# Kernel tuning notes

Hardware: AMD Instinct MI355X
Metric: run time of the kernel (lower is better)

The kernel has to match this reference:

```python
import jax, jax.numpy as jnp
import numpy as np

N_HEAD = 16
HEAD_DIM = 128

def rotate_half(x):
    x1, x2 = jnp.split(x, 2, axis=-1)
    return jnp.concatenate((-x2, x1), axis=-1)

def setup_inputs() -> dict:
    key = jax.random.key(0)
    ks = jax.random.split(key, 5)
    B, T, C = 2, 2048, 2048
    x = jax.random.normal(ks[0], (B, T, C), dtype=jnp.float32)
    # rotary tables as used by the module: cos/sin of shape [T, head_dim]
    pos = jnp.arange(T, dtype=jnp.float32)[:, None]
    inv_freq = 1.0 / (10000.0 ** (jnp.arange(0, HEAD_DIM, 2, dtype=jnp.float32) / HEAD_DIM))
    freqs = pos * inv_freq[None, :]            # [T, head_dim/2]
    emb = jnp.concatenate([freqs, freqs], -1)  # [T, head_dim]
    cos = jnp.cos(emb)
    sin = jnp.sin(emb)
    W_qkv = jax.random.normal(ks[1], (C, 3 * C), dtype=jnp.float32) * (C ** -0.5)
    W_proj = jax.random.normal(ks[2], (C, C), dtype=jnp.float32) * (C ** -0.5)
    return {"x": x, "cos": cos, "sin": sin, "W_qkv": W_qkv, "W_proj": W_proj}

def reference(x, cos, sin, W_qkv, W_proj):
    B, T, C = x.shape
    H, D = N_HEAD, HEAD_DIM
    qkv = x @ W_qkv                                   # [B,T,3C]
    q, k, v = jnp.split(qkv, 3, axis=2)
    # [B,T,C] -> [B,H,T,D]
    q = q.reshape(B, T, H, D).transpose(0, 2, 1, 3)
    k = k.reshape(B, T, H, D).transpose(0, 2, 1, 3)
    v = v.reshape(B, T, H, D).transpose(0, 2, 1, 3)
    c = cos[None, None, :, :]                          # [1,1,T,D]
    s = sin[None, None, :, :]
    q = q * c + rotate_half(q) * s
    k = k * c + rotate_half(k) * s
    scale = 1.0 / jnp.sqrt(jnp.float32(D))
    scores = jnp.einsum('bhqd,bhkd->bhqk', q, k) * scale
    attn = jax.nn.softmax(scores, axis=-1)
    y = jnp.einsum('bhqk,bhkd->bhqd', attn, v)         # [B,H,T,D]
    y = y.transpose(0, 2, 1, 3).reshape(B, T, C)
    return y @ W_proj
```

## Files before the change

### kernel.cpp

```cpp
#include <hip/hip_runtime.h>
#include <cstdint>
#include <cstddef>

typedef __bf16 bf16_t;
typedef __bf16 bf16x8 __attribute__((ext_vector_type(8)));
typedef __bf16 bf16x4 __attribute__((ext_vector_type(4)));
typedef float f32x4 __attribute__((ext_vector_type(4)));

#define MFMA16(a, b, c) __builtin_amdgcn_mfma_f32_16x16x32_bf16(a, b, c, 0, 0, 0)

__device__ __forceinline__ void gll16(const bf16_t* g, bf16_t* l) {
  __builtin_amdgcn_global_load_lds(
      (__attribute__((address_space(1))) uint32_t*)((uintptr_t)g),
      (__attribute__((address_space(3))) uint32_t*)((uint32_t)(uintptr_t)l),
      16, 0, 0);
}

__global__ void fill_diag(uint32_t* out, int n_u32) {
  int i = blockIdx.x * 256 + threadIdx.x;
  if (i < n_u32) out[i] = 0x447A0000u;
}

__global__ void conv_vec_f32(const float* __restrict__ in, bf16_t* __restrict__ out,
                             int n8) {
  const int i = blockIdx.x * 256 + threadIdx.x;
  if (i >= n8) return;
  const float* p = in + (size_t)i * 8;
  const f32x4 a = *(const f32x4*)p;
  const f32x4 b = *(const f32x4*)(p + 4);
  bf16x8 o;
#pragma unroll
  for (int j = 0; j < 4; ++j) {
    o[j] = (bf16_t)a[j];
    o[4 + j] = (bf16_t)b[j];
  }
  ((bf16x8*)out)[i] = o;
}

__global__ __launch_bounds__(256) void conv_transpose_f32(
    const float* __restrict__ in, bf16_t* __restrict__ out, int R, int C) {
  __shared__ bf16_t tile[64][72];
  const int bc = blockIdx.x * 64;
  const int br = blockIdx.y * 64;
  const int t = threadIdx.x;
  const int r = t >> 3;
  const int c8 = (t & 7) * 8;
#pragma unroll
  for (int ii = 0; ii < 2; ++ii) {
    const int rr = r + ii * 32;
    const float* p = in + (size_t)(br + rr) * C + bc + c8;
    const f32x4 a = *(const f32x4*)p;
    const f32x4 b = *(const f32x4*)(p + 4);
    bf16x8 v;
#pragma unroll
    for (int j = 0; j < 4; ++j) {
      v[j] = (bf16_t)a[j];
      v[4 + j] = (bf16_t)b[j];
    }
    *(bf16x8*)(&tile[rr][c8]) = v;
  }
  __syncthreads();
#pragma unroll
  for (int ii = 0; ii < 2; ++ii) {
    const int rr = r + ii * 32;
    bf16x8 o;
#pragma unroll
    for (int jj = 0; jj < 8; ++jj) o[jj] = tile[c8 + jj][rr];
    *(bf16x8*)(out + (size_t)(bc + rr) * R + br + c8) = o;
  }
}

#define MF8(MLO, AARR, BARR, NLO)                                           \
  do {                                                                      \
    _Pragma("unroll") for (int m_ = 0; m_ < 4; ++m_) {                      \
      _Pragma("unroll") for (int n_ = 0; n_ < 2; ++n_) {                    \
        acc[(MLO) + m_][(NLO) + n_] =                                       \
            MFMA16(AARR[m_][0], BARR[n_][0], acc[(MLO) + m_][(NLO) + n_]);  \
        acc[(MLO) + m_][(NLO) + n_] =                                       \
            MFMA16(AARR[m_][1], BARR[n_][1], acc[(MLO) + m_][(NLO) + n_]);  \
      }                                                                     \
    }                                                                       \
  } while (0)

template <bool C32>
__global__ __launch_bounds__(512, 2) void gemm8(
    const bf16_t* __restrict__ A, const bf16_t* __restrict__ Bt,
    void* __restrict__ C, int M, int N, int K, int nbn) {
  __shared__ __align__(1024) bf16_t lds8[65536];
  bf16_t* As = lds8;
  bf16_t* Bs = lds8 + 32768;

  const int tid = threadIdx.x;
  const int lane = tid & 63;
  const int wave = tid >> 6;
  const int wr = wave >> 2;
  const int wc = wave & 3;
  const int fr = lane & 15;
  const int fg = lane >> 4;

  const int nwg = gridDim.x;
  const int bid = blockIdx.x;
  const int swz = (bid & 7) * (nwg >> 3) + (bid >> 3);
  const int m0 = (swz / nbn) * 256;
  const int n0 = (swz % nbn) * 256;

  const int NT = K >> 6;

  const int sseg0 = wave * 2;
  const int srow = lane >> 3;
  const int sj = lane & 7;

  auto stage = [&](const bf16_t* __restrict__ G, int row0, bf16_t* L, int kt,
                   int h) {
#pragma unroll
    for (int l = 0; l < 2; ++l) {
      const int seg = sseg0 + l;
      const int r = seg * 8 + srow;
      const int j = sj ^ (r & 7);
      const bf16_t* src = G + (size_t)(row0 + h * 128 + r) * K + kt * 64 + j * 8;
      gll16(src, L + ((2 * kt + h) & 3) * 8192 + seg * 512 + lane * 8);
    }
  };

  const int cb0 = (fg * 16) ^ ((fr & 7) << 4);

  auto lda = [&](bf16x8(&af)[4][2], int kt, int mlo) {
    const char* base = (const char*)(As + ((2 * kt + wr) & 3) * 8192);
#pragma unroll
    for (int m = 0; m < 4; ++m) {
      const char* p = base + ((mlo + m) * 16 + fr) * 128;
      af[m][0] = *(const bf16x8*)(p + cb0);
      af[m][1] = *(const bf16x8*)(p + (cb0 ^ 64));
    }
  };
  auto ldb = [&](bf16x8(&bf)[2][2], int kt, int nlo) {
    const char* base = (const char*)(Bs + ((2 * kt + (wc >> 1)) & 3) * 8192);
#pragma unroll
    for (int n = 0; n < 2; ++n) {
      const char* p = base + ((wc & 1) * 64 + (nlo + n) * 16 + fr) * 128;
      bf[n][0] = *(const bf16x8*)(p + cb0);
      bf[n][1] = *(const bf16x8*)(p + (cb0 ^ 64));
    }
  };

  f32x4 acc[8][4] = {};

  stage(A, m0, As, 0, 0);
  stage(A, m0, As, 0, 1);
  stage(Bt, n0, Bs, 0, 0);
  stage(Bt, n0, Bs, 0, 1);
  stage(Bt, n0, Bs, 1, 0);
  stage(Bt, n0, Bs, 1, 1);
  asm volatile("s_waitcnt vmcnt(4)" ::: "memory");
  __builtin_amdgcn_s_barrier();

  bf16x8 af[4][2], bfA[2][2], bfB[2][2];

  for (int u = 0; u < NT; u += 2) {
    const bool st2 = (u + 2 < NT);
    const bool st3 = (u + 3 < NT);
    lda(af, u, 0);
    ldb(bfA, u, 0);
    stage(A, m0, As, u + 1, 0);
    asm volatile("s_waitcnt lgkmcnt(8)" ::: "memory");
    __builtin_amdgcn_s_barrier();
    asm volatile("s_waitcnt lgkmcnt(0)" ::: "memory");
    __builtin_amdgcn_sched_barrier(0);
    __builtin_amdgcn_s_setprio(1);
    MF8(0, af, bfA, 0);
    __builtin_amdgcn_s_setprio(0);
    __builtin_amdgcn_s_barrier();
    ldb(bfB, u, 2);
    stage(A, m0, As, u + 1, 1);
    __builtin_amdgcn_s_barrier();
    asm volatile("s_waitcnt lgkmcnt(0)" ::: "memory");
    __builtin_amdgcn_sched_barrier(0);
    __builtin_amdgcn_s_setprio(1);
    MF8(0, af, bfB, 2);
    __builtin_amdgcn_s_setprio(0);
    __builtin_amdgcn_s_barrier();
    lda(af, u, 4);
    if (st2) stage(Bt, n0, Bs, u + 2, 0);
    __builtin_amdgcn_s_barrier();
    asm volatile("s_waitcnt lgkmcnt(0)" ::: "memory");
    __builtin_amdgcn_sched_barrier(0);
    __builtin_amdgcn_s_setprio(1);
    MF8(4, af, bfB, 2);
    __builtin_amdgcn_s_setprio(0);
    __builtin_amdgcn_s_barrier();
    if (st2) stage(Bt, n0, Bs, u + 2, 1);
    __builtin_amdgcn_s_barrier();
    __builtin_amdgcn_s_setprio(1);
    MF8(4, af, bfA, 0);
    __builtin_amdgcn_s_setprio(0);
    asm volatile("s_waitcnt vmcnt(4)" ::: "memory");
    __builtin_amdgcn_s_barrier();
    lda(af, u + 1, 0);
    ldb(bfA, u + 1, 0);
    if (st2) stage(A, m0, As, u + 2, 0);
    asm volatile("s_waitcnt lgkmcnt(8)" ::: "memory");
    __builtin_amdgcn_s_barrier();
    asm volatile("s_waitcnt lgkmcnt(0)" ::: "memory");
    __builtin_amdgcn_sched_barrier(0);
    __builtin_amdgcn_s_setprio(1);
    MF8(0, af, bfA, 0);
    __builtin_amdgcn_s_setprio(0);
    __builtin_amdgcn_s_barrier();
    ldb(bfB, u + 1, 2);
    if (st2) stage(A, m0, As, u + 2, 1);
    __builtin_amdgcn_s_barrier();
    asm volatile("s_waitcnt lgkmcnt(0)" ::: "memory");
    __builtin_amdgcn_sched_barrier(0);
    __builtin_amdgcn_s_setprio(1);
    MF8(0, af, bfB, 2);
    __builtin_amdgcn_s_setprio(0);
    __builtin_amdgcn_s_barrier();
    lda(af, u + 1, 4);
    if (st3) stage(Bt, n0, Bs, u + 3, 0);
    __builtin_amdgcn_s_barrier();
    asm volatile("s_waitcnt lgkmcnt(0)" ::: "memory");
    __builtin_amdgcn_sched_barrier(0);
    __builtin_amdgcn_s_setprio(1);
    MF8(4, af, bfB, 2);
    __builtin_amdgcn_s_setprio(0);
    __builtin_amdgcn_s_barrier();
    if (st3) stage(Bt, n0, Bs, u + 3, 1);
    __builtin_amdgcn_s_barrier();
    __builtin_amdgcn_s_setprio(1);
    MF8(4, af, bfA, 0);
    __builtin_amdgcn_s_setprio(0);
    asm volatile("s_waitcnt vmcnt(4)" ::: "memory");
    __builtin_amdgcn_s_barrier();
  }

#pragma unroll
  for (int m = 0; m < 8; ++m) {
#pragma unroll
    for (int n = 0; n < 4; ++n) {
#pragma unroll
      for (int r = 0; r < 4; ++r) {
        const int row = m0 + wr * 128 + m * 16 + fg * 4 + r;
        const int col = n0 + wc * 64 + n * 16 + fr;
        const size_t idx = (size_t)row * N + col;
        if (C32)
          ((float*)C)[idx] = acc[m][n][r];
        else
          ((bf16_t*)C)[idx] = (bf16_t)acc[m][n][r];
      }
    }
  }
  (void)M;
}

template <bool C32>
__global__ __launch_bounds__(256) void gemm_lds(
    const bf16_t* __restrict__ A, const bf16_t* __restrict__ Bt,
    void* __restrict__ C, int M, int N, int K) {
  __shared__ __align__(16) bf16_t As[128 * 32];
  __shared__ __align__(16) bf16_t Bs[128 * 32];
  const int tid = threadIdx.x;
  const int lane = tid & 63;
  const int wave = tid >> 6;
  const int m0 = blockIdx.x * 128;
  const int n0 = blockIdx.y * 128;
  const int wm = (wave & 1) * 64;
  const int wn = (wave >> 1) * 64;
  const int fr = lane & 15;
  const int fk = (lane >> 4) * 8;

  f32x4 acc[4][4] = {};

  const bf16_t* ga = A + (size_t)(m0 + (tid >> 2)) * K + (tid & 3) * 8;
  const bf16_t* gb = Bt + (size_t)(n0 + (tid >> 2)) * K + (tid & 3) * 8;
  bf16_t* lA = As + tid * 8;
  bf16_t* lB = Bs + tid * 8;
  const size_t half = (size_t)64 * K;

  for (int k0 = 0; k0 < K; k0 += 32) {
    __syncthreads();
    gll16(ga, lA);
    gll16(ga + half, lA + 2048);
    gll16(gb, lB);
    gll16(gb + half, lB + 2048);
    ga += 32;
    gb += 32;
    __syncthreads();
    bf16x8 af[4], bfr[4];
#pragma unroll
    for (int i = 0; i < 4; ++i)
      af[i] = *(const bf16x8*)(As + (wm + i * 16 + fr) * 32 + fk);
#pragma unroll
    for (int j = 0; j < 4; ++j)
      bfr[j] = *(const bf16x8*)(Bs + (wn + j * 16 + fr) * 32 + fk);
#pragma unroll
    for (int i = 0; i < 4; ++i)
#pragma unroll
      for (int j = 0; j < 4; ++j)
        acc[i][j] = MFMA16(af[i], bfr[j], acc[i][j]);
  }

  const int fg = lane >> 4;
#pragma unroll
  for (int i = 0; i < 4; ++i) {
#pragma unroll
    for (int j = 0; j < 4; ++j) {
#pragma unroll
      for (int r = 0; r < 4; ++r) {
        const int row = m0 + wm + i * 16 + fg * 4 + r;
        const int col = n0 + wn + j * 16 + fr;
        const size_t idx = (size_t)row * N + col;
        if (C32)
          ((float*)C)[idx] = acc[i][j][r];
        else
          ((bf16_t*)C)[idx] = (bf16_t)acc[i][j][r];
      }
    }
  }
}

template <bool A32, bool C32>
__global__ __launch_bounds__(256) void gemm_t(
    const void* __restrict__ A, const bf16_t* __restrict__ Bt,
    void* __restrict__ C, int M, int N, int K) {
  __shared__ bf16_t As[128 * 32];
  __shared__ bf16_t Bs[128 * 32];
  const int tid = threadIdx.x;
  const int lane = tid & 63;
  const int wave = tid >> 6;
  const int m0 = blockIdx.x * 128;
  const int n0 = blockIdx.y * 128;
  const int wm = (wave & 1) * 64;
  const int wn = (wave >> 1) * 64;
  const int fr = lane & 15;
  const int fk = (lane >> 4) * 8;

  f32x4 acc[4][4] = {};

  const size_t ea0 = (size_t)(m0 + (tid >> 2)) * K + (tid & 3) * 8;
  const bf16_t* gb = Bt + (size_t)(n0 + (tid >> 2)) * K + (tid & 3) * 8;
  bf16_t* lA = As + tid * 8;
  bf16_t* lB = Bs + tid * 8;
  const size_t half = (size_t)64 * K;

  for (int k0 = 0; k0 < K; k0 += 32) {
    bf16x8 ra0, ra1;
    if (A32) {
      const float* pa = (const float*)A + ea0 + k0;
      const f32x4 x0 = *(const f32x4*)pa;
      const f32x4 x1 = *(const f32x4*)(pa + 4);
      const f32x4 x2 = *(const f32x4*)(pa + half);
      const f32x4 x3 = *(const f32x4*)(pa + half + 4);
#pragma unroll
      for (int j = 0; j < 4; ++j) {
        ra0[j] = (bf16_t)x0[j];
        ra0[4 + j] = (bf16_t)x1[j];
        ra1[j] = (bf16_t)x2[j];
        ra1[4 + j] = (bf16_t)x3[j];
      }
    } else {
      const bf16_t* pa = (const bf16_t*)A + ea0 + k0;
      ra0 = *(const bf16x8*)pa;
      ra1 = *(const bf16x8*)(pa + half);
    }
    const bf16x8 rb0 = *(const bf16x8*)gb;
    const bf16x8 rb1 = *(const bf16x8*)(gb + half);
    gb += 32;
    __syncthreads();
    *(bf16x8*)lA = ra0;
    *(bf16x8*)(lA + 2048) = ra1;
    *(bf16x8*)lB = rb0;
    *(bf16x8*)(lB + 2048) = rb1;
    __syncthreads();
    bf16x8 af[4], bfr[4];
#pragma unroll
    for (int i = 0; i < 4; ++i)
      af[i] = *(const bf16x8*)(As + (wm + i * 16 + fr) * 32 + fk);
#pragma unroll
    for (int j = 0; j < 4; ++j)
      bfr[j] = *(const bf16x8*)(Bs + (wn + j * 16 + fr) * 32 + fk);
#pragma unroll
    for (int i = 0; i < 4; ++i)
#pragma unroll
      for (int j = 0; j < 4; ++j)
        acc[i][j] = MFMA16(af[i], bfr[j], acc[i][j]);
  }

  const int fg = lane >> 4;
#pragma unroll
  for (int i = 0; i < 4; ++i) {
#pragma unroll
    for (int j = 0; j < 4; ++j) {
#pragma unroll
      for (int r = 0; r < 4; ++r) {
        const int row = m0 + wm + i * 16 + fg * 4 + r;
        const int col = n0 + wn + j * 16 + fr;
        const size_t idx = (size_t)row * N + col;
        if (C32)
          ((float*)C)[idx] = acc[i][j][r];
        else
          ((bf16_t*)C)[idx] = (bf16_t)acc[i][j][r];
      }
    }
  }
}

__global__ __launch_bounds__(256) void rope_k(
    const bf16_t* __restrict__ qkv, const bf16_t* __restrict__ cosb,
    const bf16_t* __restrict__ sinb, bf16_t* __restrict__ Kr) {
  const int row = blockIdx.x;
  const int t = row & 2047;
  const int b = row >> 11;
  const int idx = threadIdx.x * 8;
  const int h = idx >> 7;
  const int d = idx & 127;
  const float sgn = (d < 64) ? -1.f : 1.f;
  const bf16_t* base = qkv + (size_t)row * 6144 + 2048;
  const bf16x8 kv = *(const bf16x8*)(base + idx);
  const bf16x8 kp = *(const bf16x8*)(base + (idx ^ 64));
  const bf16x8 cv = *(const bf16x8*)(cosb + t * 128 + d);
  const bf16x8 sv = *(const bf16x8*)(sinb + t * 128 + d);
  bf16x8 o;
#pragma unroll
  for (int jj = 0; jj < 8; ++jj)
    o[jj] = (bf16_t)(((float)kv[jj]) * ((float)cv[jj]) +
                     sgn * ((float)kp[jj]) * ((float)sv[jj]));
  *(bf16x8*)(Kr + ((size_t)(b * 16 + h) * 2048 + t) * 128 + d) = o;
}

__global__ __launch_bounds__(256) void transpose_v(
    const bf16_t* __restrict__ qkv, bf16_t* __restrict__ Vt) {
  __shared__ bf16_t tile[64][72];
  const int bh = blockIdx.z;
  const int b = bh >> 4, h = bh & 15;
  const int t0 = blockIdx.x * 64;
  const int d0 = blockIdx.y * 64;
  const int t = threadIdx.x;
  const int r = t >> 3;
  const int c8 = (t & 7) * 8;
#pragma unroll
  for (int ii = 0; ii < 2; ++ii) {
    const int rr = r + ii * 32;
    *(bf16x8*)(&tile[rr][c8]) =
        *(const bf16x8*)(qkv + (size_t)(b * 2048 + t0 + rr) * 6144 + 4096 + h * 128 + d0 + c8);
  }
  __syncthreads();
#pragma unroll
  for (int ii = 0; ii < 2; ++ii) {
    const int rr = r + ii * 32;
    bf16x8 o;
#pragma unroll
    for (int jj = 0; jj < 8; ++jj) o[jj] = tile[c8 + jj][rr];
    *(bf16x8*)(Vt + ((size_t)bh * 128 + d0 + rr) * 2048 + t0 + c8) = o;
  }
}

__global__ __launch_bounds__(256) void flash_fast(
    const bf16_t* __restrict__ qkv, const bf16_t* __restrict__ cosb,
    const bf16_t* __restrict__ sinb, const bf16_t* __restrict__ Kr,
    const bf16_t* __restrict__ Vt, bf16_t* __restrict__ Y) {
  constexpr int T = 2048;
  __shared__ bf16_t Ks[64][136];
  __shared__ bf16_t Vs[128][72];
  const int tid = threadIdx.x;
  const int lane = tid & 63;
  const int wave = tid >> 6;
  const int fr = lane & 15;
  const int fg = lane >> 4;
  const int qt = blockIdx.x;
  const int bh = blockIdx.y;
  const int b = bh >> 4, h = bh & 15;

  const bf16_t* qbase = qkv + (size_t)b * T * 6144 + h * 128;
  bf16x8 qf[2][4];
#pragma unroll
  for (int i = 0; i < 2; ++i) {
    const int trow = qt * 128 + wave * 32 + i * 16 + fr;
    const bf16_t* qrow = qbase + (size_t)trow * 6144;
#pragma unroll
    for (int ks = 0; ks < 4; ++ks) {
      const int d = ks * 32 + fg * 8;
      const float sgn = (d < 64) ? -1.f : 1.f;
      const bf16x8 qv = *(const bf16x8*)(qrow + d);
      const bf16x8 qp = *(const bf16x8*)(qrow + (d ^ 64));
      const bf16x8 cv = *(const bf16x8*)(cosb + trow * 128 + d);
      const bf16x8 sv = *(const bf16x8*)(sinb + trow * 128 + d);
      bf16x8 o;
#pragma unroll
      for (int jj = 0; jj < 8; ++jj)
        o[jj] = (bf16_t)((((float)qv[jj]) * ((float)cv[jj]) +
                          sgn * ((float)qp[jj]) * ((float)sv[jj])) *
                         0.1275174825f);
      qf[i][ks] = o;
    }
  }

  f32x4 acc[2][8] = {};
  float l_i[2] = {0.f, 0.f};

  const int krow = tid >> 4;
  const int kcol = (tid & 15) * 8;
  const int vrow = tid >> 3;
  const int vu = tid & 7;
  const int vc0 = ((vu >> 2) * 32) + ((vu & 1) * 16) + (((vu >> 1) & 1) * 4);
  const bf16_t* Kh = Kr + (size_t)bh * T * 128;
  const bf16_t* Vh = Vt + (size_t)bh * 128 * T;

  bf16x8 kreg[4], vreg[4];
  auto load_kv = [&](int t0) {
#pragma unroll
    for (int it = 0; it < 4; ++it)
      kreg[it] = *(const bf16x8*)(Kh + (size_t)(t0 + it * 16 + krow) * 128 + kcol);
#pragma unroll
    for (int it = 0; it < 4; ++it)
      vreg[it] = *(const bf16x8*)(Vh + (size_t)(it * 32 + vrow) * T + t0 + vu * 8);
  };

  load_kv(0);

  for (int j = 0; j < T / 64; ++j) {
#pragma unroll
    for (int it = 0; it < 4; ++it)
      *(bf16x8*)(&Ks[it * 16 + krow][kcol]) = kreg[it];
#pragma unroll
    for (int it = 0; it < 4; ++it) {
      const int row = it * 32 + vrow;
      const bf16x8 v = vreg[it];
      bf16x4 lo, hi;
#pragma unroll
      for (int jj = 0; jj < 4; ++jj) {
        lo[jj] = v[jj];
        hi[jj] = v[4 + jj];
      }
      *(bf16x4*)(&Vs[row][vc0]) = lo;
      *(bf16x4*)(&Vs[row][vc0 + 8]) = hi;
    }
    __syncthreads();

    f32x4 sacc[2][4] = {};
#pragma unroll
    for (int n = 0; n < 4; ++n) {
#pragma unroll
      for (int ks = 0; ks < 4; ++ks) {
        const bf16x8 kf = *(const bf16x8*)(&Ks[n * 16 + fr][ks * 32 + fg * 8]);
        sacc[0][n] = MFMA16(kf, qf[0][ks], sacc[0][n]);
        sacc[1][n] = MFMA16(kf, qf[1][ks], sacc[1][n]);
      }
    }

    if (j + 1 < T / 64) load_kv((j + 1) * 64);

    bf16x8 paf[2][2];
#pragma unroll
    for (int i = 0; i < 2; ++i) {
      float lsum = 0.f;
#pragma unroll
      for (int ks2 = 0; ks2 < 2; ++ks2) {
#pragma unroll
        for (int jj = 0; jj < 8; ++jj) {
          const float p = exp2f(sacc[i][ks2 * 2 + (jj >> 2)][jj & 3]);
          lsum += p;
          paf[i][ks2][jj] = (bf16_t)p;
        }
      }
      l_i[i] += lsum;
    }

#pragma unroll
    for (int ks2 = 0; ks2 < 2; ++ks2) {
#pragma unroll
      for (int n = 0; n < 8; ++n) {
        const bf16x8 vf = *(const bf16x8*)(&Vs[n * 16 + fr][ks2 * 32 + fg * 8]);
        acc[0][n] = MFMA16(paf[0][ks2], vf, acc[0][n]);
        acc[1][n] = MFMA16(paf[1][ks2], vf, acc[1][n]);
      }
    }
    __syncthreads();
  }

#pragma unroll
  for (int i = 0; i < 2; ++i) {
    float l = l_i[i];
    l += __shfl_xor(l, 16, 64);
    l += __shfl_xor(l, 32, 64);
#pragma unroll
    for (int r = 0; r < 4; ++r) {
      const float inv = 1.0f / __shfl(l, fg * 4 + r, 64);
      const int t = qt * 128 + wave * 32 + i * 16 + fg * 4 + r;
      bf16_t* yrow = Y + (size_t)(b * T + t) * 2048 + h * 128;
#pragma unroll
      for (int n = 0; n < 8; ++n)
        yrow[n * 16 + fr] = (bf16_t)(acc[i][n][r] * inv);
    }
  }
}

__global__ __launch_bounds__(256) void flash_fused_v2(
    const bf16_t* __restrict__ qkv, const bf16_t* __restrict__ cosb,
    const bf16_t* __restrict__ sinb, bf16_t* __restrict__ Y) {
  constexpr int T = 2048;
  __shared__ bf16_t Ks[64][136];
  __shared__ bf16_t Vs[128][72];
  __shared__ bf16_t Ps[128][72];
  const int tid = threadIdx.x;
  const int lane = tid & 63;
  const int wave = tid >> 6;
  const int fr = lane & 15;
  const int fg = lane >> 4;
  const int qt = blockIdx.x;
  const int bh = blockIdx.y;
  const int b = bh >> 4, h = bh & 15;

  const bf16_t* qbase = qkv + (size_t)b * T * 6144 + h * 128;
  bf16x8 qf[2][4];
#pragma unroll
  for (int i = 0; i < 2; ++i) {
    const int trow = qt * 128 + wave * 32 + i * 16 + fr;
    const bf16_t* qrow = qbase + (size_t)trow * 6144;
#pragma unroll
    for (int ks = 0; ks < 4; ++ks) {
      const int d = ks * 32 + fg * 8;
      const float sgn = (d < 64) ? -1.f : 1.f;
      const bf16x8 qv = *(const bf16x8*)(qrow + d);
      const bf16x8 qp = *(const bf16x8*)(qrow + (d ^ 64));
      const bf16x8 cv = *(const bf16x8*)(cosb + trow * 128 + d);
      const bf16x8 sv = *(const bf16x8*)(sinb + trow * 128 + d);
      bf16x8 o;
#pragma unroll
      for (int jj = 0; jj < 8; ++jj)
        o[jj] = (bf16_t)((((float)qv[jj]) * ((float)cv[jj]) +
                          sgn * ((float)qp[jj]) * ((float)sv[jj])) *
                         0.08838834764831845f);
      qf[i][ks] = o;
    }
  }

  f32x4 acc[2][8] = {};
  float l_i[2][4] = {};

  const int kr = tid >> 4;
  const int kc = (tid & 15) * 8;
  const float sgnk = (kc < 64) ? -1.f : 1.f;
  const int tp = tid & 63;

  for (int j = 0; j < T / 64; ++j) {
    const int t0 = j * 64;
#pragma unroll
    for (int it = 0; it < 4; ++it) {
      const int row = it * 16 + kr;
      const int tg = t0 + row;
      const bf16_t* krow = qkv + ((size_t)(b * T + tg)) * 6144 + 2048 + h * 128;
      const bf16x8 kv = *(const bf16x8*)(krow + kc);
      const bf16x8 kp = *(const bf16x8*)(krow + (kc ^ 64));
      const bf16x8 cv = *(const bf16x8*)(cosb + tg * 128 + kc);
      const bf16x8 sv = *(const bf16x8*)(sinb + tg * 128 + kc);
      bf16x8 o;
#pragma unroll
      for (int jj = 0; jj < 8; ++jj)
        o[jj] = (bf16_t)(((float)kv[jj]) * ((float)cv[jj]) +
                         sgnk * ((float)kp[jj]) * ((float)sv[jj]));
      *(bf16x8*)(&Ks[row][kc]) = o;
    }
#pragma unroll
    for (int cc = 0; cc < 4; ++cc) {
      const int d8 = (cc * 4 + (tid >> 6)) * 8;
      const bf16x8 vv = *(const bf16x8*)(qkv + ((size_t)(b * T + t0 + tp)) * 6144 +
                                         4096 + h * 128 + d8);
#pragma unroll
      for (int jj = 0; jj < 8; ++jj) Vs[d8 + jj][tp] = vv[jj];
    }
    __syncthreads();

    f32x4 sacc[2][4] = {};
#pragma unroll
    for (int n = 0; n < 4; ++n) {
#pragma unroll
      for (int ks = 0; ks < 4; ++ks) {
        const bf16x8 kf = *(const bf16x8*)(&Ks[n * 16 + fr][ks * 32 + fg * 8]);
        sacc[0][n] = MFMA16(qf[0][ks], kf, sacc[0][n]);
        sacc[1][n] = MFMA16(qf[1][ks], kf, sacc[1][n]);
      }
    }

#pragma unroll
    for (int i = 0; i < 2; ++i) {
#pragma unroll
      for (int r = 0; r < 4; ++r) {
        const float p0 = __expf(sacc[i][0][r]);
        const float p1 = __expf(sacc[i][1][r]);
        const float p2 = __expf(sacc[i][2][r]);
        const float p3 = __expf(sacc[i][3][r]);
        l_i[i][r] += (p0 + p1) + (p2 + p3);
        const int prow = wave * 32 + i * 16 + fg * 4 + r;
        Ps[prow][0 + fr] = (bf16_t)p0;
        Ps[prow][16 + fr] = (bf16_t)p1;
        Ps[prow][32 + fr] = (bf16_t)p2;
        Ps[prow][48 + fr] = (bf16_t)p3;
      }
    }

#pragma unroll
    for (int ks = 0; ks < 2; ++ks) {
      const bf16x8 pf0 = *(const bf16x8*)(&Ps[wave * 32 + fr][ks * 32 + fg * 8]);
      const bf16x8 pf1 = *(const bf16x8*)(&Ps[wave * 32 + 16 + fr][ks * 32 + fg * 8]);
#pragma unroll
      for (int n = 0; n < 8; ++n) {
        const bf16x8 vf = *(const bf16x8*)(&Vs[n * 16 + fr][ks * 32 + fg * 8]);
        acc[0][n] = MFMA16(pf0, vf, acc[0][n]);
        acc[1][n] = MFMA16(pf1, vf, acc[1][n]);
      }
    }
    __syncthreads();
  }

#pragma unroll
  for (int i = 0; i < 2; ++i) {
#pragma unroll
    for (int r = 0; r < 4; ++r) {
      float l = l_i[i][r];
#pragma unroll
      for (int msk = 1; msk < 16; msk <<= 1) l += __shfl_xor(l, msk, 64);
      const float inv = 1.0f / l;
      const int t = qt * 128 + wave * 32 + i * 16 + fg * 4 + r;
      bf16_t* yrow = Y + (size_t)(b * T + t) * 2048 + h * 128;
#pragma unroll
      for (int n = 0; n < 8; ++n)
        yrow[n * 16 + fr] = (bf16_t)(acc[i][n][r] * inv);
    }
  }
}

extern "C" void kernel_launch(void* const* d_in, const int* in_sizes, int n_in,
                              void* d_out, int out_size, void* d_ws, size_t ws_size,
                              hipStream_t stream) {
  const float* x = (const float*)d_in[0];
  const float* cosi = (const float*)d_in[1];
  const float* sini = (const float*)d_in[2];
  const float* Wqkv = (const float*)d_in[3];
  const float* Wproj = (const float*)d_in[4];

  const size_t NEED_FAST = sizeof(bf16_t) *
      ((size_t)12582912 + 262144 + 262144 + 25165824 + 8388608 + 8388608);
  const size_t NEED_BASE = 256 + sizeof(bf16_t) *
      ((size_t)12582912 + 4194304 + 262144 + 262144 + 25165824);

  if (ws_size >= NEED_FAST) {
    bf16_t* base = (bf16_t*)d_ws;
    bf16_t* WqkvT = base;
    bf16_t* y = base;
    bf16_t* cosb = base + 12582912;
    bf16_t* sinb = cosb + 262144;
    bf16_t* qkv = sinb + 262144;
    bf16_t* WprojT = qkv;
    bf16_t* Kr = qkv + 25165824;
    bf16_t* xb = Kr;
    bf16_t* Vt = Kr + 8388608;

    conv_vec_f32<<<128, 256, 0, stream>>>(cosi, cosb, 32768);
    conv_vec_f32<<<128, 256, 0, stream>>>(sini, sinb, 32768);
    conv_vec_f32<<<4096, 256, 0, stream>>>(x, xb, 1048576);
    conv_transpose_f32<<<dim3(96, 32), 256, 0, stream>>>(Wqkv, WqkvT, 2048, 6144);
    gemm8<false><<<384, 512, 0, stream>>>(xb, WqkvT, qkv, 4096, 6144, 2048, 24);
    rope_k<<<4096, 256, 0, stream>>>(qkv, cosb, sinb, Kr);
    transpose_v<<<dim3(32, 2, 32), 256, 0, stream>>>(qkv, Vt);
    flash_fast<<<dim3(16, 32), 256, 0, stream>>>(qkv, cosb, sinb, Kr, Vt, y);
    conv_transpose_f32<<<dim3(32, 32), 256, 0, stream>>>(Wproj, WprojT, 2048, 2048);
    gemm_lds<true><<<dim3(32, 16), 256, 0, stream>>>(y, WprojT, d_out, 4096, 2048, 2048);
  } else if (ws_size >= NEED_BASE) {
    bf16_t* base = (bf16_t*)((char*)d_ws + 256);
    bf16_t* WqkvT = base;
    bf16_t* y = base;
    bf16_t* WprojT = base + 12582912;
    bf16_t* cosb = WprojT + 4194304;
    bf16_t* sinb = cosb + 262144;
    bf16_t* qkv = sinb + 262144;

    conv_vec_f32<<<128, 256, 0, stream>>>(cosi, cosb, 32768);
    conv_vec_f32<<<128, 256, 0, stream>>>(sini, sinb, 32768);
    conv_transpose_f32<<<dim3(96, 32), 256, 0, stream>>>(Wqkv, WqkvT, 2048, 6144);
    gemm_t<true, false><<<dim3(32, 48), 256, 0, stream>>>(x, WqkvT, qkv, 4096, 6144, 2048);
    flash_fused_v2<<<dim3(16, 32), 256, 0, stream>>>(qkv, cosb, sinb, y);
    conv_transpose_f32<<<dim3(32, 32), 256, 0, stream>>>(Wproj, WprojT, 2048, 2048);
    gemm_t<false, true><<<dim3(32, 16), 256, 0, stream>>>(y, WprojT, d_out, 4096, 2048, 2048);
  } else {
    fill_diag<<<(out_size + 255) / 256, 256, 0, stream>>>((uint32_t*)d_out, out_size);
  }
}
```

Before: 471.6 us.

## Stream K/V fragments from global memory in flash kernel, dropping LDS staging

Replaces the LDS-staged, register-prefetched K/V tiles in the flash attention kernel with direct per-wave global loads of MFMA fragments. This removes both block barriers and the LDS writes per tile, and sets launch bounds to encourage two blocks per CU. In exchange, every wave reloads the same K/V data through the cache hierarchy, V is fetched with narrower 8-byte loads, and the software prefetch overlap is lost.

```diff
diff --git a/kernel.cpp b/kernel.cpp
--- a/kernel.cpp
+++ b/kernel.cpp
@@ -454,13 +454,11 @@
   }
 }
 
-__global__ __launch_bounds__(256) void flash_fast(
+__global__ __launch_bounds__(256, 2) void flash_stream(
     const bf16_t* __restrict__ qkv, const bf16_t* __restrict__ cosb,
     const bf16_t* __restrict__ sinb, const bf16_t* __restrict__ Kr,
     const bf16_t* __restrict__ Vt, bf16_t* __restrict__ Y) {
   constexpr int T = 2048;
-  __shared__ bf16_t Ks[64][136];
-  __shared__ bf16_t Vs[128][72];
   const int tid = threadIdx.x;
   const int lane = tid & 63;
   const int wave = tid >> 6;
@@ -497,57 +495,22 @@
   f32x4 acc[2][8] = {};
   float l_i[2] = {0.f, 0.f};
 
-  const int krow = tid >> 4;
-  const int kcol = (tid & 15) * 8;
-  const int vrow = tid >> 3;
-  const int vu = tid & 7;
-  const int vc0 = ((vu >> 2) * 32) + ((vu & 1) * 16) + (((vu >> 1) & 1) * 4);
-  const bf16_t* Kh = Kr + (size_t)bh * T * 128;
-  const bf16_t* Vh = Vt + (size_t)bh * 128 * T;
-
-  bf16x8 kreg[4], vreg[4];
-  auto load_kv = [&](int t0) {
-#pragma unroll
-    for (int it = 0; it < 4; ++it)
-      kreg[it] = *(const bf16x8*)(Kh + (size_t)(t0 + it * 16 + krow) * 128 + kcol);
-#pragma unroll
-    for (int it = 0; it < 4; ++it)
-      vreg[it] = *(const bf16x8*)(Vh + (size_t)(it * 32 + vrow) * T + t0 + vu * 8);
-  };
-
-  load_kv(0);
+  const bf16_t* Kh = Kr + (size_t)bh * T * 128 + (size_t)fr * 128 + fg * 8;
+  const bf16_t* Vh = Vt + (size_t)bh * 128 * T + (size_t)fr * T + fg * 4;
 
   for (int j = 0; j < T / 64; ++j) {
-#pragma unroll
-    for (int it = 0; it < 4; ++it)
-      *(bf16x8*)(&Ks[it * 16 + krow][kcol]) = kreg[it];
-#pragma unroll
-    for (int it = 0; it < 4; ++it) {
-      const int row = it * 32 + vrow;
-      const bf16x8 v = vreg[it];
-      bf16x4 lo, hi;
-#pragma unroll
-      for (int jj = 0; jj < 4; ++jj) {
-        lo[jj] = v[jj];
-        hi[jj] = v[4 + jj];
-      }
-      *(bf16x4*)(&Vs[row][vc0]) = lo;
-      *(bf16x4*)(&Vs[row][vc0 + 8]) = hi;
-    }
-    __syncthreads();
-
+    const int t0 = j * 64;
     f32x4 sacc[2][4] = {};
 #pragma unroll
     for (int n = 0; n < 4; ++n) {
+      const bf16_t* krow = Kh + (size_t)(t0 + n * 16) * 128;
 #pragma unroll
       for (int ks = 0; ks < 4; ++ks) {
-        const bf16x8 kf = *(const bf16x8*)(&Ks[n * 16 + fr][ks * 32 + fg * 8]);
+        const bf16x8 kf = *(const bf16x8*)(krow + ks * 32);
         sacc[0][n] = MFMA16(kf, qf[0][ks], sacc[0][n]);
         sacc[1][n] = MFMA16(kf, qf[1][ks], sacc[1][n]);
       }
     }
-
-    if (j + 1 < T / 64) load_kv((j + 1) * 64);
 
     bf16x8 paf[2][2];
 #pragma unroll
@@ -569,12 +532,14 @@
     for (int ks2 = 0; ks2 < 2; ++ks2) {
 #pragma unroll
       for (int n = 0; n < 8; ++n) {
-        const bf16x8 vf = *(const bf16x8*)(&Vs[n * 16 + fr][ks2 * 32 + fg * 8]);
+        const bf16_t* vrow = Vh + (size_t)(n * 16) * T + t0 + ks2 * 32;
+        const bf16x4 lo = *(const bf16x4*)(vrow);
+        const bf16x4 hi = *(const bf16x4*)(vrow + 16);
+        const bf16x8 vf = __builtin_shufflevector(lo, hi, 0, 1, 2, 3, 4, 5, 6, 7);
         acc[0][n] = MFMA16(paf[0][ks2], vf, acc[0][n]);
         acc[1][n] = MFMA16(paf[1][ks2], vf, acc[1][n]);
       }
     }
-    __syncthreads();
   }
 
 #pragma unroll
@@ -762,7 +727,7 @@
     gemm8<false><<<384, 512, 0, stream>>>(xb, WqkvT, qkv, 4096, 6144, 2048, 24);
     rope_k<<<4096, 256, 0, stream>>>(qkv, cosb, sinb, Kr);
     transpose_v<<<dim3(32, 2, 32), 256, 0, stream>>>(qkv, Vt);
-    flash_fast<<<dim3(16, 32), 256, 0, stream>>>(qkv, cosb, sinb, Kr, Vt, y);
+    flash_stream<<<dim3(16, 32), 256, 0, stream>>>(qkv, cosb, sinb, Kr, Vt, y);
     conv_transpose_f32<<<dim3(32, 32), 256, 0, stream>>>(Wproj, WprojT, 2048, 2048);
     gemm_lds<true><<<dim3(32, 16), 256, 0, stream>>>(y, WprojT, d_out, 4096, 2048, 2048);
   } else if (ws_size >= NEED_BASE) {
```

After: 693.3 us. +47.0%, slower.

## Halve query tile per block to 64 rows and raise flash occupancy

Applied to the files above, without the earlier changes.

The flash kernel now gives each wave 16 query rows instead of 32, and each block 64 instead of 128. The grid doubles to 1024 blocks and the launch bound asks for 4 blocks per SM, cutting per-thread accumulator registers so more waves are resident. The register prefetch of the next K/V tile is dropped, and global loads now go straight into LDS each iteration. The cost is that K/V tiles are reloaded twice as often per query row, with less compute per sync and no software pipelining.

```diff
diff --git a/kernel.cpp b/kernel.cpp
--- a/kernel.cpp
+++ b/kernel.cpp
@@ -454,7 +454,7 @@
   }
 }
 
-__global__ __launch_bounds__(256) void flash_fast(
+__global__ __launch_bounds__(256, 4) void flash_q64(
     const bf16_t* __restrict__ qkv, const bf16_t* __restrict__ cosb,
     const bf16_t* __restrict__ sinb, const bf16_t* __restrict__ Kr,
     const bf16_t* __restrict__ Vt, bf16_t* __restrict__ Y) {
@@ -470,32 +470,28 @@
   const int bh = blockIdx.y;
   const int b = bh >> 4, h = bh & 15;
 
-  const bf16_t* qbase = qkv + (size_t)b * T * 6144 + h * 128;
-  bf16x8 qf[2][4];
-#pragma unroll
-  for (int i = 0; i < 2; ++i) {
-    const int trow = qt * 128 + wave * 32 + i * 16 + fr;
-    const bf16_t* qrow = qbase + (size_t)trow * 6144;
-#pragma unroll
-    for (int ks = 0; ks < 4; ++ks) {
-      const int d = ks * 32 + fg * 8;
-      const float sgn = (d < 64) ? -1.f : 1.f;
-      const bf16x8 qv = *(const bf16x8*)(qrow + d);
-      const bf16x8 qp = *(const bf16x8*)(qrow + (d ^ 64));
-      const bf16x8 cv = *(const bf16x8*)(cosb + trow * 128 + d);
-      const bf16x8 sv = *(const bf16x8*)(sinb + trow * 128 + d);
-      bf16x8 o;
-#pragma unroll
-      for (int jj = 0; jj < 8; ++jj)
-        o[jj] = (bf16_t)((((float)qv[jj]) * ((float)cv[jj]) +
-                          sgn * ((float)qp[jj]) * ((float)sv[jj])) *
-                         0.1275174825f);
-      qf[i][ks] = o;
-    }
-  }
-
-  f32x4 acc[2][8] = {};
-  float l_i[2] = {0.f, 0.f};
+  const int trow = qt * 64 + wave * 16 + fr;
+  const bf16_t* qrow = qkv + (size_t)(b * T + trow) * 6144 + h * 128;
+  bf16x8 qf[4];
+#pragma unroll
+  for (int ks = 0; ks < 4; ++ks) {
+    const int d = ks * 32 + fg * 8;
+    const float sgn = (d < 64) ? -1.f : 1.f;
+    const bf16x8 qv = *(const bf16x8*)(qrow + d);
+    const bf16x8 qp = *(const bf16x8*)(qrow + (d ^ 64));
+    const bf16x8 cv = *(const bf16x8*)(cosb + trow * 128 + d);
+    const bf16x8 sv = *(const bf16x8*)(sinb + trow * 128 + d);
+    bf16x8 o;
+#pragma unroll
+    for (int jj = 0; jj < 8; ++jj)
+      o[jj] = (bf16_t)((((float)qv[jj]) * ((float)cv[jj]) +
+                        sgn * ((float)qp[jj]) * ((float)sv[jj])) *
+                       0.1275174825f);
+    qf[ks] = o;
+  }
+
+  f32x4 acc[8] = {};
+  float l_i = 0.f;
 
   const int krow = tid >> 4;
   const int kcol = (tid & 15) * 8;
@@ -505,26 +501,16 @@
   const bf16_t* Kh = Kr + (size_t)bh * T * 128;
   const bf16_t* Vh = Vt + (size_t)bh * 128 * T;
 
-  bf16x8 kreg[4], vreg[4];
-  auto load_kv = [&](int t0) {
+  for (int j = 0; j < T / 64; ++j) {
+    const int t0 = j * 64;
 #pragma unroll
     for (int it = 0; it < 4; ++it)
-      kreg[it] = *(const bf16x8*)(Kh + (size_t)(t0 + it * 16 + krow) * 128 + kcol);
-#pragma unroll
-    for (int it = 0; it < 4; ++it)
-      vreg[it] = *(const bf16x8*)(Vh + (size_t)(it * 32 + vrow) * T + t0 + vu * 8);
-  };
-
-  load_kv(0);
-
-  for (int j = 0; j < T / 64; ++j) {
-#pragma unroll
-    for (int it = 0; it < 4; ++it)
-      *(bf16x8*)(&Ks[it * 16 + krow][kcol]) = kreg[it];
+      *(bf16x8*)(&Ks[it * 16 + krow][kcol]) =
+          *(const bf16x8*)(Kh + (size_t)(t0 + it * 16 + krow) * 128 + kcol);
 #pragma unroll
     for (int it = 0; it < 4; ++it) {
       const int row = it * 32 + vrow;
-      const bf16x8 v = vreg[it];
+      const bf16x8 v = *(const bf16x8*)(Vh + (size_t)row * T + t0 + vu * 8);
       bf16x4 lo, hi;
 #pragma unroll
       for (int jj = 0; jj < 4; ++jj) {
@@ -536,61 +522,51 @@
     }
     __syncthreads();
 
-    f32x4 sacc[2][4] = {};
+    f32x4 sacc[4] = {};
 #pragma unroll
     for (int n = 0; n < 4; ++n) {
 #pragma unroll
       for (int ks = 0; ks < 4; ++ks) {
         const bf16x8 kf = *(const bf16x8*)(&Ks[n * 16 + fr][ks * 32 + fg * 8]);
-        sacc[0][n] = MFMA16(kf, qf[0][ks], sacc[0][n]);
-        sacc[1][n] = MFMA16(kf, qf[1][ks], sacc[1][n]);
-      }
-    }
-
-    if (j + 1 < T / 64) load_kv((j + 1) * 64);
-
-    bf16x8 paf[2][2];
-#pragma unroll
-    for (int i = 0; i < 2; ++i) {
-      float lsum = 0.f;
-#pragma unroll
-      for (int ks2 = 0; ks2 < 2; ++ks2) {
-#pragma unroll
-        for (int jj = 0; jj < 8; ++jj) {
-          const float p = exp2f(sacc[i][ks2 * 2 + (jj >> 2)][jj & 3]);
-          lsum += p;
-          paf[i][ks2][jj] = (bf16_t)p;
-        }
-      }
-      l_i[i] += lsum;
-    }
+        sacc[n] = MFMA16(kf, qf[ks], sacc[n]);
+      }
+    }
+
+    bf16x8 paf[2];
+    float lsum = 0.f;
+#pragma unroll
+    for (int ks2 = 0; ks2 < 2; ++ks2) {
+#pragma unroll
+      for (int jj = 0; jj < 8; ++jj) {
+        const float p = exp2f(sacc[ks2 * 2 + (jj >> 2)][jj & 3]);
+        lsum += p;
+        paf[ks2][jj] = (bf16_t)p;
+      }
+    }
+    l_i += lsum;
 
 #pragma unroll
     for (int ks2 = 0; ks2 < 2; ++ks2) {
 #pragma unroll
       for (int n = 0; n < 8; ++n) {
         const bf16x8 vf = *(const bf16x8*)(&Vs[n * 16 + fr][ks2 * 32 + fg * 8]);
-        acc[0][n] = MFMA16(paf[0][ks2], vf, acc[0][n]);
-        acc[1][n] = MFMA16(paf[1][ks2], vf, acc[1][n]);
+        acc[n] = MFMA16(paf[ks2], vf, acc[n]);
       }
     }
     __syncthreads();
   }
 
-#pragma unroll
-  for (int i = 0; i < 2; ++i) {
-    float l = l_i[i];
-    l += __shfl_xor(l, 16, 64);
-    l += __shfl_xor(l, 32, 64);
-#pragma unroll
-    for (int r = 0; r < 4; ++r) {
-      const float inv = 1.0f / __shfl(l, fg * 4 + r, 64);
-      const int t = qt * 128 + wave * 32 + i * 16 + fg * 4 + r;
-      bf16_t* yrow = Y + (size_t)(b * T + t) * 2048 + h * 128;
-#pragma unroll
-      for (int n = 0; n < 8; ++n)
-        yrow[n * 16 + fr] = (bf16_t)(acc[i][n][r] * inv);
-    }
+  float l = l_i;
+  l += __shfl_xor(l, 16, 64);
+  l += __shfl_xor(l, 32, 64);
+#pragma unroll
+  for (int r = 0; r < 4; ++r) {
+    const float inv = 1.0f / __shfl(l, fg * 4 + r, 64);
+    const int t = qt * 64 + wave * 16 + fg * 4 + r;
+    bf16_t* yrow = Y + (size_t)(b * T + t) * 2048 + h * 128;
+#pragma unroll
+    for (int n = 0; n < 8; ++n)
+      yrow[n * 16 + fr] = (bf16_t)(acc[n][r] * inv);
   }
 }
 
@@ -762,7 +738,7 @@
     gemm8<false><<<384, 512, 0, stream>>>(xb, WqkvT, qkv, 4096, 6144, 2048, 24);
     rope_k<<<4096, 256, 0, stream>>>(qkv, cosb, sinb, Kr);
     transpose_v<<<dim3(32, 2, 32), 256, 0, stream>>>(qkv, Vt);
-    flash_fast<<<dim3(16, 32), 256, 0, stream>>>(qkv, cosb, sinb, Kr, Vt, y);
+    flash_q64<<<dim3(32, 32), 256, 0, stream>>>(qkv, cosb, sinb, Kr, Vt, y);
     conv_transpose_f32<<<dim3(32, 32), 256, 0, stream>>>(Wproj, WprojT, 2048, 2048);
     gemm_lds<true><<<dim3(32, 16), 256, 0, stream>>>(y, WprojT, d_out, 4096, 2048, 2048);
   } else if (ws_size >= NEED_BASE) {
```

After: 457.7 us. 1.03x faster.
